# Kernel tuning notes

Hardware: AMD Instinct MI355X
Metric: run time of the kernel (lower is better)

## Reference

```python
import jax, jax.numpy as jnp
import numpy as np

B, N, C = 8, 2048, 256

def setup_inputs() -> dict:
    key = jax.random.key(0)
    ks = jax.random.split(key, 6)
    corr = jax.random.normal(ks[0], (B, N, N), dtype=jnp.float32)
    feat = jax.random.normal(ks[1], (B, N, C), dtype=jnp.float32)
    histogram = jax.random.uniform(ks[2], (B, N, 1), dtype=jnp.float32)
    mask = jax.random.normal(ks[3], (N, N), dtype=jnp.float32)
    # nn.Linear(C, C) params
    lim = 1.0 / np.sqrt(C)
    v_w = jax.random.uniform(ks[4], (C, C), minval=-lim, maxval=lim, dtype=jnp.float32)
    v_b = jax.random.uniform(ks[5], (C,), minval=-lim, maxval=lim, dtype=jnp.float32)
    return {"corr": corr, "feat": feat, "histogram": histogram, "mask": mask, "v_w": v_w, "v_b": v_b}

def reference(corr, feat, histogram, mask, v_w, v_b):
    # histogram is viewed/expanded in the original but never used downstream.
    # masked softmax over last axis: (b, n, n)
    attn = jax.nn.softmax(corr + mask[None, :, :], axis=-1)
    # v projection: y = feat @ v_w.T + v_b   (b, n, c)
    ref_feat_v = jnp.einsum("bnc,dc->bnd", feat, v_w) + v_b
    # attention output: (b, n, c)
    return jnp.einsum("bnm,bmc->bnc", attn, ref_feat_v)
```

## Files before the change

### kernel.cpp

```cpp
#include <hip/hip_runtime.h>
#include <hip/hip_fp16.h>


#define B_ 8
#define N_ 2048
#define C_ 256

typedef _Float16 half8  __attribute__((ext_vector_type(8)));
typedef _Float16 half4v __attribute__((ext_vector_type(4)));
typedef float    f32x4  __attribute__((ext_vector_type(4)));

__global__ __launch_bounds__(256) void k_convw(const float* __restrict__ w,
                                               _Float16* __restrict__ wh) {
    int i = (blockIdx.x * 256 + threadIdx.x) * 4;
    float4 v = *(const float4*)(w + i);
    half4v h = {(_Float16)v.x, (_Float16)v.y, (_Float16)v.z, (_Float16)v.w};
    *(half4v*)(wh + i) = h;
}

__global__ __launch_bounds__(256) void k_trans(const float* __restrict__ feat,
                                               _Float16* __restrict__ featF) {
    __shared__ _Float16 s[64][68];
    int blk  = blockIdx.x;
    int b    = blk >> 7;
    int tile = blk & 127;
    int n0   = (tile >> 2) << 6;
    int c0   = (tile & 3) << 6;
    int t    = threadIdx.x;

    const float* src = feat + ((size_t)(b * N_ + n0)) * C_ + c0;
#pragma unroll
    for (int i = 0; i < 4; ++i) {
        int idx = i * 256 + t;
        int row = idx >> 4;
        int c4  = (idx & 15) << 2;
        float4 v = *(const float4*)(src + (size_t)row * C_ + c4);
        half4v h = {(_Float16)v.x, (_Float16)v.y, (_Float16)v.z, (_Float16)v.w};
        *(half4v*)&s[row][c4] = h;
    }
    __syncthreads();

    int w = t >> 6, l = t & 63;
    int kk  = w & 1;
    int cb0 = (w >> 1) << 1;
#pragma unroll
    for (int cbi = 0; cbi < 2; ++cbi) {
        int cb = cb0 + cbi;
        half8 v;
#pragma unroll
        for (int j = 0; j < 8; ++j)
            v[j] = s[kk * 32 + ((l >> 4) << 3) + j][(cb << 4) + (l & 15)];
        _Float16* dst = featF +
            (((size_t)((b * 64 + (n0 >> 5) + kk) * 16 + (c0 >> 4) + cb)) * 64 + l) * 8;
        *(half8*)dst = v;
    }
}

__global__ __launch_bounds__(512, 4) void k_attn(const float* __restrict__ corr,
                                                 const float* __restrict__ mask,
                                                 const _Float16* __restrict__ featF,
                                                 _Float16* __restrict__ T) {
    __shared__ _Float16 p_lds[2][32 * 64];
    __shared__ float rowsum[32];

    const int rblk = blockIdx.x >> 3;
    const int b    = blockIdx.x & 7;
    const int r0   = rblk * 32;
    const int tg   = threadIdx.x;
    const int w    = tg >> 6, l = tg & 63;
    const int lrow = l & 15, kch = l >> 4;

    const int srow = tg >> 4;
    const int scol = (tg & 15) << 2;

    const float*    pc  = corr + ((size_t)(b * N_ + r0 + srow)) * N_ + scol;
    const float*    pm  = mask + ((size_t)(r0 + srow)) * N_ + scol;
    const _Float16* pfb = featF + (size_t)b * (64 * 16 * 512);

    const int swaddr = srow * 64 + (((scol >> 3) ^ (srow & 7)) << 3) + (scol & 7);
    const int ag0 = ((kch ^ (lrow & 7)) << 3);
    const int ag1 = (((4 + kch) ^ (lrow & 7)) << 3);

    float rs = 0.0f;
    f32x4 acc[2][2] = {};

#define EXPSTORE(TT, CC, MM)                                                  \
    {                                                                         \
        float p0 = __expf((CC).x + (MM).x), p1 = __expf((CC).y + (MM).y);     \
        float p2 = __expf((CC).z + (MM).z), p3 = __expf((CC).w + (MM).w);     \
        rs += (p0 + p1) + (p2 + p3);                                          \
        half4v h = {(_Float16)p0, (_Float16)p1, (_Float16)p2, (_Float16)p3};  \
        *(half4v*)&p_lds[(TT) & 1][swaddr] = h;                               \
    }

    float4 cP = *(const float4*)pc;
    float4 mP = *(const float4*)pm;
    float4 cA = *(const float4*)(pc + 64);
    float4 mA = *(const float4*)(pm + 64);
    float4 cB, mB;
    EXPSTORE(0, cP, mP);
    __syncthreads();

#define STEP(T_, CCON, MCON, CLD, MLD)                                        \
    {                                                                         \
        const int t_ = (T_);                                                  \
        if (t_ < 30) {                                                        \
            CLD = *(const float4*)(pc + (t_ + 2) * 64);                       \
            MLD = *(const float4*)(pm + (t_ + 2) * 64);                       \
        }                                                                     \
        {                                                                     \
            const _Float16* pl = &p_lds[t_ & 1][0];                           \
            _Pragma("unroll")                                                 \
            for (int kk = 0; kk < 2; ++kk) {                                  \
                const int gofs = kk ? ag1 : ag0;                              \
                half8 a0 = *(const half8*)&pl[lrow * 64 + gofs];              \
                half8 a1 = *(const half8*)&pl[(16 + lrow) * 64 + gofs];       \
                const _Float16* pf =                                          \
                    pfb + (((size_t)((2 * t_ + kk) * 16 + w * 2)) * 64 + l) * 8; \
                half8 b0 = *(const half8*)pf;                                 \
                half8 b1 = *(const half8*)(pf + 512);                         \
                acc[0][0] = __builtin_amdgcn_mfma_f32_16x16x32_f16(a0, b0, acc[0][0], 0, 0, 0); \
                acc[0][1] = __builtin_amdgcn_mfma_f32_16x16x32_f16(a0, b1, acc[0][1], 0, 0, 0); \
                acc[1][0] = __builtin_amdgcn_mfma_f32_16x16x32_f16(a1, b0, acc[1][0], 0, 0, 0); \
                acc[1][1] = __builtin_amdgcn_mfma_f32_16x16x32_f16(a1, b1, acc[1][1], 0, 0, 0); \
            }                                                                 \
        }                                                                     \
        if (t_ < 31) EXPSTORE(t_ + 1, CCON, MCON);                            \
        asm volatile("s_waitcnt lgkmcnt(0)" ::: "memory");                    \
        __builtin_amdgcn_sched_barrier(0);                                    \
        __builtin_amdgcn_s_barrier();                                         \
        __builtin_amdgcn_sched_barrier(0);                                    \
    }

    for (int th = 0; th < 16; ++th) {
        STEP(2 * th,     cA, mA, cB, mB);
        STEP(2 * th + 1, cB, mB, cA, mA);
    }
#undef STEP
#undef EXPSTORE

    rs += __shfl_xor(rs, 1);
    rs += __shfl_xor(rs, 2);
    rs += __shfl_xor(rs, 4);
    rs += __shfl_xor(rs, 8);
    if ((l & 15) == 0) rowsum[srow] = rs;
    __syncthreads();

#pragma unroll
    for (int m = 0; m < 2; ++m) {
        float inv[4];
#pragma unroll
        for (int j = 0; j < 4; ++j)
            inv[j] = 1.0f / rowsum[m * 16 + kch * 4 + j];
        _Float16* pT = T + ((size_t)(b * N_ + r0 + m * 16 + kch * 4)) * C_
                         + w * 32 + lrow;
#pragma unroll
        for (int j = 0; j < 4; ++j) {
#pragma unroll
            for (int n = 0; n < 2; ++n) {
                pT[(size_t)j * C_ + n * 16] = (_Float16)(acc[m][n][j] * inv[j]);
            }
        }
    }
}

__global__ __launch_bounds__(256, 2) void k_out(const _Float16* __restrict__ T,
                                                const _Float16* __restrict__ wh,
                                                const float* __restrict__ v_b,
                                                float* __restrict__ out) {
    const int blk = blockIdx.x;
    const int r0  = blk * 32;
    const int t   = threadIdx.x;
    const int w   = t >> 6, l = t & 63;
    const int wr  = w >> 1, wc = w & 1;
    const int lrow = l & 15, kch = l >> 4;

    const _Float16* pA = T  + ((size_t)(r0 + wr * 16 + lrow)) * C_ + kch * 8;
    const _Float16* pB = wh + ((size_t)(wc * 128 + lrow)) * C_ + kch * 8;

    f32x4 acc[8] = {};
#pragma unroll
    for (int step = 0; step < 8; step++) {
        half8 a = *(const half8*)(pA + step * 32);
#pragma unroll
        for (int q = 0; q < 8; q++) {
            half8 bf = *(const half8*)(pB + step * 32 + (size_t)q * 16 * C_);
            acc[q] = __builtin_amdgcn_mfma_f32_16x16x32_f16(a, bf, acc[q], 0, 0, 0);
        }
    }

    float* pO = out + ((size_t)(r0 + wr * 16 + kch * 4)) * C_ + wc * 128 + lrow;
#pragma unroll
    for (int q = 0; q < 8; q++) {
        float bias = v_b[wc * 128 + q * 16 + lrow];
#pragma unroll
        for (int j = 0; j < 4; j++) {
            pO[(size_t)j * C_ + q * 16] = acc[q][j] + bias;
        }
    }
}

extern "C" void kernel_launch(void* const* d_in, const int* in_sizes, int n_in,
                              void* d_out, int out_size, void* d_ws, size_t ws_size,
                              hipStream_t stream) {
    const float* corr = (const float*)d_in[0];
    const float* feat = (const float*)d_in[1];
    const float* mask = (const float*)d_in[3];
    const float* v_w  = (const float*)d_in[4];
    const float* v_b  = (const float*)d_in[5];
    float* out = (float*)d_out;

    char* ws = (char*)d_ws;
    _Float16* featF = (_Float16*)ws;
    _Float16* T     = (_Float16*)(ws + (size_t)8 * 1024 * 1024);
    _Float16* wh    = (_Float16*)(ws + (size_t)16 * 1024 * 1024);

    hipLaunchKernelGGL(k_trans, dim3(1024), dim3(256), 0, stream, feat, featF);
    hipLaunchKernelGGL(k_convw, dim3(64),   dim3(256), 0, stream, v_w, wh);
    hipLaunchKernelGGL(k_attn,  dim3(512),  dim3(512), 0, stream, corr, mask, featF, T);
    hipLaunchKernelGGL(k_out,   dim3(512),  dim3(256), 0, stream, T, wh, v_b, out);
}
```

Measured before the change: 76.40 us.

## Make attention waves independent with per-wave softmax tiles and no block barriers

Restructures k_attn so each wave owns 16 rows and half of the channels, computing exp(corr+mask) into its own private LDS double buffer. This removes the block-wide s_barrier every k-step and the shared rowsum sync. Each block now covers 64 rows, so the grid halves and launch bounds drop to 2 blocks per CU. The tradeoff is that each pair of waves recomputes the same exp tile and loads the same corr/mask data, doubling those loads and exp work. Register pressure also rises (8 accumulators, 16 B fragments, 24 float4 prefetch registers), which could hurt occupancy.

```diff
diff --git a/kernel.cpp b/kernel.cpp
--- a/kernel.cpp
+++ b/kernel.cpp
@@ -56,80 +56,107 @@
     }
 }
 
-__global__ __launch_bounds__(512, 4) void k_attn(const float* __restrict__ corr,
+__global__ __launch_bounds__(512, 2) void k_attn(const float* __restrict__ corr,
                                                  const float* __restrict__ mask,
                                                  const _Float16* __restrict__ featF,
                                                  _Float16* __restrict__ T) {
-    __shared__ _Float16 p_lds[2][32 * 64];
-    __shared__ float rowsum[32];
-
-    const int rblk = blockIdx.x >> 3;
-    const int b    = blockIdx.x & 7;
-    const int r0   = rblk * 32;
-    const int tg   = threadIdx.x;
-    const int w    = tg >> 6, l = tg & 63;
+    __shared__ _Float16 p_lds[8][2][16 * 64];
+    __shared__ float rowsum[8][16];
+
+    const int rg = blockIdx.x >> 3;
+    const int b  = blockIdx.x & 7;
+    const int tg = threadIdx.x;
+    const int w  = tg >> 6, l = tg & 63;
+    const int ch = w & 1;
+    const int r0 = rg * 64 + (w >> 1) * 16;
     const int lrow = l & 15, kch = l >> 4;
 
-    const int srow = tg >> 4;
-    const int scol = (tg & 15) << 2;
-
-    const float*    pc  = corr + ((size_t)(b * N_ + r0 + srow)) * N_ + scol;
-    const float*    pm  = mask + ((size_t)(r0 + srow)) * N_ + scol;
-    const _Float16* pfb = featF + (size_t)b * (64 * 16 * 512);
-
-    const int swaddr = srow * 64 + (((scol >> 3) ^ (srow & 7)) << 3) + (scol & 7);
+    const int srow = l >> 4;
+    const int scol = (l & 15) << 2;
+
+    const float* pc = corr + ((size_t)(b * N_ + r0 + srow)) * N_ + scol;
+    const float* pm = mask + ((size_t)(r0 + srow)) * N_ + scol;
+    const _Float16* pw = featF + (size_t)b * 524288 + ch * 4096 + l * 8;
+
+    _Float16* const pl0 = &p_lds[w][0][0];
+    _Float16* const pl1 = &p_lds[w][1][0];
+
+    int wad[4];
+#pragma unroll
+    for (int q = 0; q < 4; ++q) {
+        int row = q * 4 + srow;
+        wad[q] = row * 64 + (((scol >> 3) ^ (row & 7)) << 3) + (scol & 7);
+    }
+    const int rA  = lrow * 64;
     const int ag0 = ((kch ^ (lrow & 7)) << 3);
     const int ag1 = (((4 + kch) ^ (lrow & 7)) << 3);
 
-    float rs = 0.0f;
-    f32x4 acc[2][2] = {};
-
-#define EXPSTORE(TT, CC, MM)                                                  \
+    float rs[4] = {0.f, 0.f, 0.f, 0.f};
+    f32x4 acc[8] = {};
+
+#define EXPSTORE(BUF, CC, MM)                                                 \
     {                                                                         \
-        float p0 = __expf((CC).x + (MM).x), p1 = __expf((CC).y + (MM).y);     \
-        float p2 = __expf((CC).z + (MM).z), p3 = __expf((CC).w + (MM).w);     \
-        rs += (p0 + p1) + (p2 + p3);                                          \
-        half4v h = {(_Float16)p0, (_Float16)p1, (_Float16)p2, (_Float16)p3};  \
-        *(half4v*)&p_lds[(TT) & 1][swaddr] = h;                               \
-    }
-
-    float4 cP = *(const float4*)pc;
-    float4 mP = *(const float4*)pm;
-    float4 cA = *(const float4*)(pc + 64);
-    float4 mA = *(const float4*)(pm + 64);
-    float4 cB, mB;
+        _Float16* pld = (BUF) ? pl1 : pl0;                                    \
+        _Pragma("unroll")                                                     \
+        for (int q = 0; q < 4; ++q) {                                         \
+            float p0 = __expf((CC)[q].x + (MM)[q].x);                         \
+            float p1 = __expf((CC)[q].y + (MM)[q].y);                         \
+            float p2 = __expf((CC)[q].z + (MM)[q].z);                         \
+            float p3 = __expf((CC)[q].w + (MM)[q].w);                         \
+            rs[q] += (p0 + p1) + (p2 + p3);                                   \
+            half4v h = {(_Float16)p0, (_Float16)p1, (_Float16)p2, (_Float16)p3}; \
+            *(half4v*)&pld[wad[q]] = h;                                       \
+        }                                                                     \
+        asm volatile("s_waitcnt lgkmcnt(0)" ::: "memory");                    \
+        __builtin_amdgcn_sched_barrier(0);                                    \
+    }
+
+    float4 cP[4], mP[4], cA[4], mA[4], cB[4], mB[4];
+#pragma unroll
+    for (int q = 0; q < 4; ++q) {
+        cP[q] = *(const float4*)(pc + (size_t)q * 4 * N_);
+        mP[q] = *(const float4*)(pm + (size_t)q * 4 * N_);
+    }
+#pragma unroll
+    for (int q = 0; q < 4; ++q) {
+        cA[q] = *(const float4*)(pc + (size_t)q * 4 * N_ + 64);
+        mA[q] = *(const float4*)(pm + (size_t)q * 4 * N_ + 64);
+    }
     EXPSTORE(0, cP, mP);
-    __syncthreads();
 
 #define STEP(T_, CCON, MCON, CLD, MLD)                                        \
     {                                                                         \
         const int t_ = (T_);                                                  \
+                                              \
         if (t_ < 30) {                                                        \
-            CLD = *(const float4*)(pc + (t_ + 2) * 64);                       \
-            MLD = *(const float4*)(pm + (t_ + 2) * 64);                       \
-        }                                                                     \
-        {                                                                     \
-            const _Float16* pl = &p_lds[t_ & 1][0];                           \
             _Pragma("unroll")                                                 \
-            for (int kk = 0; kk < 2; ++kk) {                                  \
-                const int gofs = kk ? ag1 : ag0;                              \
-                half8 a0 = *(const half8*)&pl[lrow * 64 + gofs];              \
-                half8 a1 = *(const half8*)&pl[(16 + lrow) * 64 + gofs];       \
-                const _Float16* pf =                                          \
-                    pfb + (((size_t)((2 * t_ + kk) * 16 + w * 2)) * 64 + l) * 8; \
-                half8 b0 = *(const half8*)pf;                                 \
-                half8 b1 = *(const half8*)(pf + 512);                         \
-                acc[0][0] = __builtin_amdgcn_mfma_f32_16x16x32_f16(a0, b0, acc[0][0], 0, 0, 0); \
-                acc[0][1] = __builtin_amdgcn_mfma_f32_16x16x32_f16(a0, b1, acc[0][1], 0, 0, 0); \
-                acc[1][0] = __builtin_amdgcn_mfma_f32_16x16x32_f16(a1, b0, acc[1][0], 0, 0, 0); \
-                acc[1][1] = __builtin_amdgcn_mfma_f32_16x16x32_f16(a1, b1, acc[1][1], 0, 0, 0); \
+            for (int q = 0; q < 4; ++q) {                                     \
+                CLD[q] = *(const float4*)(pc + (size_t)q * 4 * N_ + (t_ + 2) * 64); \
+                MLD[q] = *(const float4*)(pm + (size_t)q * 4 * N_ + (t_ + 2) * 64); \
             }                                                                 \
         }                                                                     \
-        if (t_ < 31) EXPSTORE(t_ + 1, CCON, MCON);                            \
-        asm volatile("s_waitcnt lgkmcnt(0)" ::: "memory");                    \
-        __builtin_amdgcn_sched_barrier(0);                                    \
-        __builtin_amdgcn_s_barrier();                                         \
-        __builtin_amdgcn_sched_barrier(0);                                    \
+             \
+        half8 bf[2][8];                                                       \
+        _Pragma("unroll")                                                     \
+        for (int kk = 0; kk < 2; ++kk) {                                      \
+            _Pragma("unroll")                                                 \
+            for (int n = 0; n < 8; ++n)                                       \
+                bf[kk][n] = *(const half8*)(pw + (size_t)t_ * 16384           \
+                                               + kk * 8192 + n * 512);        \
+        }                                                                     \
+           \
+        const _Float16* pl = (t_ & 1) ? pl1 : pl0;                            \
+        half8 a0 = *(const half8*)&pl[rA + ag0];                              \
+        half8 a1 = *(const half8*)&pl[rA + ag1];                              \
+              \
+        if (t_ < 31) EXPSTORE((t_ + 1) & 1, CCON, MCON);                      \
+                                                                   \
+        _Pragma("unroll")                                                     \
+        for (int n = 0; n < 8; ++n)                                           \
+            acc[n] = __builtin_amdgcn_mfma_f32_16x16x32_f16(a0, bf[0][n], acc[n], 0, 0, 0); \
+        _Pragma("unroll")                                                     \
+        for (int n = 0; n < 8; ++n)                                           \
+            acc[n] = __builtin_amdgcn_mfma_f32_16x16x32_f16(a1, bf[1][n], acc[n], 0, 0, 0); \
     }
 
     for (int th = 0; th < 16; ++th) {
@@ -139,27 +166,29 @@
 #undef STEP
 #undef EXPSTORE
 
-    rs += __shfl_xor(rs, 1);
-    rs += __shfl_xor(rs, 2);
-    rs += __shfl_xor(rs, 4);
-    rs += __shfl_xor(rs, 8);
-    if ((l & 15) == 0) rowsum[srow] = rs;
-    __syncthreads();
-
-#pragma unroll
-    for (int m = 0; m < 2; ++m) {
-        float inv[4];
-#pragma unroll
-        for (int j = 0; j < 4; ++j)
-            inv[j] = 1.0f / rowsum[m * 16 + kch * 4 + j];
-        _Float16* pT = T + ((size_t)(b * N_ + r0 + m * 16 + kch * 4)) * C_
-                         + w * 32 + lrow;
-#pragma unroll
-        for (int j = 0; j < 4; ++j) {
-#pragma unroll
-            for (int n = 0; n < 2; ++n) {
-                pT[(size_t)j * C_ + n * 16] = (_Float16)(acc[m][n][j] * inv[j]);
-            }
+#pragma unroll
+    for (int q = 0; q < 4; ++q) {
+        rs[q] += __shfl_xor(rs[q], 1);
+        rs[q] += __shfl_xor(rs[q], 2);
+        rs[q] += __shfl_xor(rs[q], 4);
+        rs[q] += __shfl_xor(rs[q], 8);
+    }
+    if ((l & 15) == 0) {
+#pragma unroll
+        for (int q = 0; q < 4; ++q) rowsum[w][q * 4 + srow] = rs[q];
+    }
+    asm volatile("s_waitcnt lgkmcnt(0)" ::: "memory");
+    __builtin_amdgcn_sched_barrier(0);
+    float inv[4];
+#pragma unroll
+    for (int j = 0; j < 4; ++j) inv[j] = 1.0f / rowsum[w][kch * 4 + j];
+
+    _Float16* pT = T + ((size_t)(b * N_ + r0 + kch * 4)) * C_ + ch * 128 + lrow;
+#pragma unroll
+    for (int j = 0; j < 4; ++j) {
+#pragma unroll
+        for (int n = 0; n < 8; ++n) {
+            pT[(size_t)j * C_ + n * 16] = (_Float16)(acc[n][j] * inv[j]);
         }
     }
 }
@@ -217,6 +246,6 @@
 
     hipLaunchKernelGGL(k_trans, dim3(1024), dim3(256), 0, stream, feat, featF);
     hipLaunchKernelGGL(k_convw, dim3(64),   dim3(256), 0, stream, v_w, wh);
-    hipLaunchKernelGGL(k_attn,  dim3(512),  dim3(512), 0, stream, corr, mask, featF, T);
+    hipLaunchKernelGGL(k_attn,  dim3(256),  dim3(512), 0, stream, corr, mask, featF, T);
     hipLaunchKernelGGL(k_out,   dim3(512),  dim3(256), 0, stream, T, wh, v_b, out);
 }
```

Result: slower. 96.27 us (+26.0%).
